# Kernel tuning notes

Hardware: AMD Instinct MI355X
Metric: run time of the kernel (lower is better)

Reference implementation:

```python
import jax, jax.numpy as jnp
import numpy as np

N = 100000      # nodes per node type (A and B)
D = 128         # input feature dim
H = 128         # hidden_size
E = 1600000     # edges per message type (avg degree 16)
P_DROP = 0.2
# message types (src, ei, dst): (A, ei0, A), (A, ei1, B), (B, ei2, A)


def setup_inputs() -> dict:
    key = jax.random.key(0)
    ks = jax.random.split(key, 16)
    s = 0.02
    inp = {
        "xA": jax.random.normal(ks[0], (N, D), jnp.float32),
        "xB": jax.random.normal(ks[1], (N, D), jnp.float32),
        "ei0": jax.random.randint(ks[2], (2, E), 0, N),
        "ei1": jax.random.randint(ks[3], (2, E), 0, N),
        "ei2": jax.random.randint(ks[4], (2, E), 0, N),
        "Wn1": jax.random.normal(ks[5], (3, D, H), jnp.float32) * s,
        "Ws1": jax.random.normal(ks[6], (3, D, H), jnp.float32) * s,
        "Wu1": jax.random.normal(ks[7], (3, 2 * H, H), jnp.float32) * s,
        "Wn2": jax.random.normal(ks[8], (3, H, H), jnp.float32) * s,
        "Ws2": jax.random.normal(ks[9], (3, H, H), jnp.float32) * s,
        "Wu2": jax.random.normal(ks[10], (3, 2 * H, H), jnp.float32) * s,
    }
    for name in ["bn1", "bs1", "bu1", "bn2", "bs2", "bu2"]:
        inp[name] = jnp.zeros((3, H), jnp.float32)
    return inp


def _dropout(x, key):
    # F.dropout(training=True) with a fixed key for determinism
    keep = jax.random.bernoulli(key, 1.0 - P_DROP, x.shape)
    return jnp.where(keep, x / (1.0 - P_DROP), jnp.zeros((), x.dtype))


def _segment_mean(msgs, dst, num_segments):
    # scatter-mean aggregation; isolated nodes get 0 (PyG 'mean' aggr)
    s = jax.ops.segment_sum(msgs, dst, num_segments=num_segments)
    cnt = jax.ops.segment_sum(jnp.ones((dst.shape[0], 1), msgs.dtype), dst,
                              num_segments=num_segments)
    return s / jnp.maximum(cnt, 1.0)


def _sage(x_src, x_dst, ei, Wn, bn, Ws, bs, Wu, bu):
    # HeteroSAGEConv: mean-aggregate neighbor feats, then
    # lin_update(cat(lin_neigh(aggr), lin_self(x_dst)))
    aggr = _segment_mean(x_src[ei[0]], ei[1], x_dst.shape[0])  # [N_dst, D]
    h = jnp.concatenate([aggr @ Wn + bn, x_dst @ Ws + bs], axis=-1)
    return h @ Wu + bu


def _hetero_layer(xA, xB, ei0, ei1, ei2, Wn, bn, Ws, bs, Wu, bu):
    # HeteroConv: sum per-message-type conv outputs sharing the same dst type
    oA = (_sage(xA, xA, ei0, Wn[0], bn[0], Ws[0], bs[0], Wu[0], bu[0])
          + _sage(xB, xA, ei2, Wn[2], bn[2], Ws[2], bs[2], Wu[2], bu[2]))
    oB = _sage(xA, xB, ei1, Wn[1], bn[1], Ws[1], bs[1], Wu[1], bu[1])
    return oA, oB


def reference(xA, xB, ei0, ei1, ei2,
              Wn1, bn1, Ws1, bs1, Wu1, bu1,
              Wn2, bn2, Ws2, bs2, Wu2, bu2):
    dk = jax.random.split(jax.random.key(42), 4)
    hA = jax.nn.relu(_dropout(xA, dk[0]))
    hB = jax.nn.relu(_dropout(xB, dk[1]))
    hA, hB = _hetero_layer(hA, hB, ei0, ei1, ei2, Wn1, bn1, Ws1, bs1, Wu1, bu1)
    hA = jax.nn.relu(_dropout(hA, dk[2]))
    hB = jax.nn.relu(_dropout(hB, dk[3]))
    return _hetero_layer(hA, hB, ei0, ei1, ei2, Wn2, bn2, Ws2, bs2, Wu2, bu2)
```

## Files before the change

kernel.cpp:

```cpp
#include <hip/hip_runtime.h>
#include <cstdint>
#include <cstdio>

#define DIMF 128
#define BKT_SHIFT 9
#define BKT_MAX 1024
#define P1_CHUNK 8192
#define P1_CAP 16384
#define P2_CAP 12288

typedef __attribute__((ext_vector_type(8))) short short8v;
typedef __attribute__((ext_vector_type(4))) short short4v;
typedef __attribute__((ext_vector_type(4))) float f32x4;


__host__ __device__ __forceinline__ void tf2x32(uint32_t k0, uint32_t k1,
                                                uint32_t x0, uint32_t x1,
                                                uint32_t& o0, uint32_t& o1) {
  uint32_t ks2 = k0 ^ k1 ^ 0x1BD11BDAu;
  x0 += k0; x1 += k1;
#define TFR(r) { x0 += x1; x1 = (x1 << (r)) | (x1 >> (32 - (r))); x1 ^= x0; }
  TFR(13) TFR(15) TFR(26) TFR(6)
  x0 += k1;  x1 += ks2 + 1u;
  TFR(17) TFR(29) TFR(16) TFR(24)
  x0 += ks2; x1 += k0 + 2u;
  TFR(13) TFR(15) TFR(26) TFR(6)
  x0 += k0;  x1 += k1 + 3u;
  TFR(17) TFR(29) TFR(16) TFR(24)
  x0 += k1;  x1 += ks2 + 4u;
  TFR(13) TFR(15) TFR(26) TFR(6)
  x0 += ks2; x1 += k0 + 5u;
#undef TFR
  o0 = x0; o1 = x1;
}

__device__ __forceinline__ short f2bf_rne(float x) {
  uint32_t u = __float_as_uint(x);
  uint32_t r = (u + 0x7FFFu + ((u >> 16) & 1u)) >> 16;
  return (short)r;
}
__device__ __forceinline__ float bfhi_f(short h) {
  return __uint_as_float(((uint32_t)(uint16_t)h) << 16);
}
__device__ __forceinline__ void unpk2(uint32_t w, float& f0, float& f1) {
  f0 = __uint_as_float(w << 16);
  f1 = __uint_as_float(w & 0xFFFF0000u);
}

__global__ __launch_bounds__(256) void k_drop2(const float* __restrict__ xA,
                                               const float* __restrict__ xB,
                                               uint32_t* __restrict__ hiA, uint32_t* __restrict__ loA,
                                               uint32_t* __restrict__ hiB, uint32_t* __restrict__ loB,
                                               int npair, int gdrop,
                                               uint32_t ka0, uint32_t ka1,
                                               uint32_t kb0, uint32_t kb1) {
  int isB = blockIdx.x >= gdrop;
  int p = (blockIdx.x - (isB ? gdrop : 0)) * 256 + threadIdx.x;
  if (p >= npair) return;
  const float* in = isB ? xB : xA;
  uint32_t* hiP = isB ? hiB : hiA;
  uint32_t* loP = isB ? loB : loA;
  uint32_t k0 = isB ? kb0 : ka0, k1 = isB ? kb1 : ka1;
  int row = p >> 6, w = p & 63;
  int c2 = w * 2;
  float2 x = *(const float2*)(in + (size_t)row * 128 + c2);
  uint32_t idx = (uint32_t)(row * 128 + c2);
  float v[2] = {x.x, x.y};
  uint32_t hw = 0, lw = 0;
#pragma unroll
  for (int q = 0; q < 2; ++q) {
    uint32_t o0, o1;
    tf2x32(k0, k1, 0u, idx + q, o0, o1);
    uint32_t bits = o0 ^ o1;
    float u = __uint_as_float((bits >> 9) | 0x3f800000u) - 1.0f;
    float y = (u < 0.8f) ? (v[q] / 0.8f) : 0.0f;
    y = fmaxf(y, 0.0f);
    short hi = f2bf_rne(y);
    short lo = f2bf_rne(y - bfhi_f(hi));
    hw |= (uint32_t)(uint16_t)hi << (16 * q);
    lw |= (uint32_t)(uint16_t)lo << (16 * q);
  }
  hiP[(size_t)row * 64 + w] = hw;
  loP[(size_t)row * 64 + w] = lw;
}

__global__ __launch_bounds__(256) void k_ginit(int* __restrict__ gcur, int nbk) {
  for (int i = threadIdx.x; i < nbk; i += 256) gcur[i] = i * P1_CAP;
}

__global__ __launch_bounds__(256) void k_p1(const int* __restrict__ ei0,
                                            const int* __restrict__ ei1,
                                            const int* __restrict__ ei2,
                                            int* __restrict__ gcur,
                                            uint32_t* __restrict__ p1o,
                                            int E, int n, int gE8, int nbk) {
  __shared__ int hist[BKT_MAX];
  __shared__ int cur[BKT_MAX];
  int t = threadIdx.x;
  int type = blockIdx.x / gE8;
  int chunk = blockIdx.x - type * gE8;
  const int* ei = type == 0 ? ei0 : (type == 1 ? ei1 : ei2);
  int base = chunk * P1_CHUNK;
  int dof = type * n;
  for (int i = t; i < nbk; i += 256) hist[i] = 0;
  __syncthreads();
  int sv[P1_CHUNK / 256];
  int dv[P1_CHUNK / 256];
#pragma unroll
  for (int j = 0; j < P1_CHUNK / 256; ++j) {
    int e = base + j * 256 + t;
    if (e < E) { sv[j] = ei[e]; dv[j] = ei[E + e] + dof; }
    else dv[j] = -1;
  }
#pragma unroll
  for (int j = 0; j < P1_CHUNK / 256; ++j)
    if (dv[j] >= 0) atomicAdd(&hist[dv[j] >> BKT_SHIFT], 1);
  __syncthreads();
  for (int i = t; i < nbk; i += 256) {
    int h = hist[i];
    if (h > 0) cur[i] = atomicAdd(&gcur[i], h);
  }
  __syncthreads();
#pragma unroll
  for (int j = 0; j < P1_CHUNK / 256; ++j) {
    if (dv[j] >= 0) {
      int bkt = dv[j] >> BKT_SHIFT;
      int pos = atomicAdd(&cur[bkt], 1);
      p1o[pos] = (uint32_t)sv[j] | ((uint32_t)(dv[j] & 511) << 20);
    }
  }
}

__global__ __launch_bounds__(256) void k_bscan2(const int* __restrict__ gcur,
                                                int* __restrict__ boff,
                                                int* __restrict__ off,
                                                int nbk, int n3) {
  __shared__ int ts[256];
  int t = threadIdx.x;
  int base = t * 4;
  int v[4];
#pragma unroll
  for (int i = 0; i < 4; ++i)
    v[i] = (base + i < nbk) ? (gcur[base + i] - (base + i) * P1_CAP) : 0;
  ts[t] = v[0] + v[1] + v[2] + v[3];
  __syncthreads();
  for (int ofs = 1; ofs < 256; ofs <<= 1) {
    int x = ts[t];
    int y = (t >= ofs) ? ts[t - ofs] : 0;
    __syncthreads();
    ts[t] = x + y;
    __syncthreads();
  }
  int run = (t == 0) ? 0 : ts[t - 1];
#pragma unroll
  for (int i = 0; i < 4; ++i) {
    if (base + i < nbk) boff[base + i] = run;
    run += v[i];
  }
  if (t == 255) { boff[nbk] = ts[255]; off[n3] = ts[255]; }
}

__global__ __launch_bounds__(256) void k_p2(const uint32_t* __restrict__ p1o,
                                            const int* __restrict__ boff,
                                            int* __restrict__ off,
                                            int* __restrict__ srcl, int n3) {
  __shared__ int cnt_l[512];
  __shared__ int off_l[512];
  __shared__ int cur_l[512];
  __shared__ int ts[256];
  __shared__ int img[P2_CAP];
  int b = blockIdx.x;
  int t = threadIdx.x;
  int fb = boff[b];
  int sz = boff[b + 1] - fb;
  size_t pb = (size_t)b * P1_CAP;
  int d0 = b << BKT_SHIFT;
  cnt_l[t] = 0; cnt_l[t + 256] = 0;
  __syncthreads();
  for (int i = t; i < sz; i += 256)
    atomicAdd(&cnt_l[p1o[pb + i] >> 20], 1);
  __syncthreads();
  int c0 = cnt_l[2 * t], c1 = cnt_l[2 * t + 1];
  ts[t] = c0 + c1;
  __syncthreads();
  for (int ofs = 1; ofs < 256; ofs <<= 1) {
    int x = ts[t];
    int y = (t >= ofs) ? ts[t - ofs] : 0;
    __syncthreads();
    ts[t] = x + y;
    __syncthreads();
  }
  int ebase = (t == 0) ? 0 : ts[t - 1];
  off_l[2 * t] = ebase; off_l[2 * t + 1] = ebase + c0;
  cur_l[2 * t] = ebase; cur_l[2 * t + 1] = ebase + c0;
  __syncthreads();
  for (int j = t; j < 512; j += 256) {
    int d = d0 + j;
    if (d < n3) off[d] = fb + off_l[j];
  }
  if (sz <= P2_CAP) {
    for (int i = t; i < sz; i += 256) {
      uint32_t w = p1o[pb + i];
      int pos = atomicAdd(&cur_l[w >> 20], 1);
      img[pos] = (int)(w & 0xFFFFFu) << 6;
    }
    __syncthreads();
    for (int i = t; i < sz; i += 256) srcl[fb + i] = img[i];
  } else {
    for (int i = t; i < sz; i += 256) {
      uint32_t w = p1o[pb + i];
      int pos = atomicAdd(&cur_l[w >> 20], 1);
      srcl[fb + pos] = (int)(w & 0xFFFFFu) << 6;
    }
  }
}

__device__ __forceinline__ void gather_one32(const uint32_t* __restrict__ hiP,
                                             const int* __restrict__ off,
                                             const int* __restrict__ srcl,
                                             short* __restrict__ out,
                                             int d, int lane) {
  int b = off[d], e = off[d + 1];
  const int c2 = lane * 2;
  float a0 = 0.f, a1 = 0.f, a2 = 0.f, a3 = 0.f;
  float b0 = 0.f, b1 = 0.f, b2 = 0.f, b3 = 0.f;
  float c0 = 0.f, c1 = 0.f, c2f = 0.f, c3 = 0.f;
  float e0 = 0.f, e1 = 0.f, e2 = 0.f, e3 = 0.f;
  float t0, t1;
  int j = b;
  for (; j + 3 < e; j += 4) {
    int o0 = __builtin_nontemporal_load(srcl + j);
    int o1 = __builtin_nontemporal_load(srcl + j + 1);
    int o2 = __builtin_nontemporal_load(srcl + j + 2);
    int o3 = __builtin_nontemporal_load(srcl + j + 3);
    uint2 w0 = *(const uint2*)(hiP + (size_t)(o0 + c2));
    uint2 w1 = *(const uint2*)(hiP + (size_t)(o1 + c2));
    uint2 w2 = *(const uint2*)(hiP + (size_t)(o2 + c2));
    uint2 w3 = *(const uint2*)(hiP + (size_t)(o3 + c2));
    unpk2(w0.x, t0, t1); a0 += t0; a1 += t1;
    unpk2(w0.y, t0, t1); a2 += t0; a3 += t1;
    unpk2(w1.x, t0, t1); b0 += t0; b1 += t1;
    unpk2(w1.y, t0, t1); b2 += t0; b3 += t1;
    unpk2(w2.x, t0, t1); c0 += t0; c1 += t1;
    unpk2(w2.y, t0, t1); c2f += t0; c3 += t1;
    unpk2(w3.x, t0, t1); e0 += t0; e1 += t1;
    unpk2(w3.y, t0, t1); e2 += t0; e3 += t1;
  }
  for (; j < e; ++j) {
    int o = __builtin_nontemporal_load(srcl + j);
    uint2 w = *(const uint2*)(hiP + (size_t)(o + c2));
    unpk2(w.x, t0, t1); a0 += t0; a1 += t1;
    unpk2(w.y, t0, t1); a2 += t0; a3 += t1;
  }
  float sc = 1.0f / (float)max(e - b, 1);
  short4v r = { f2bf_rne(((a0 + b0) + (c0 + e0)) * sc),
                f2bf_rne(((a1 + b1) + (c1 + e1)) * sc),
                f2bf_rne(((a2 + b2) + (c2f + e2)) * sc),
                f2bf_rne(((a3 + b3) + (c3 + e3)) * sc) };
  __builtin_nontemporal_store(r, (short4v*)(out + (size_t)d * 128 + lane * 4));
}

__global__ __launch_bounds__(256) void k_gather3(
    const uint32_t* __restrict__ hiA, const uint32_t* __restrict__ hiB,
    short* __restrict__ g1, short* __restrict__ g2, short* __restrict__ g3,
    const int* __restrict__ off, const int* __restrict__ srcl, int n) {
  int wv = (blockIdx.x * 256 + threadIdx.x) >> 6;
  int half = (threadIdx.x >> 5) & 1;
  int lane = threadIdx.x & 31;
  int d = wv * 2 + half;
  if (d >= 3 * n) return;
  if (d < n)          gather_one32(hiA, off + n,     srcl, g1, d,         lane);
  else if (d < 2 * n) gather_one32(hiB, off + 2 * n, srcl, g2, d - n,     lane);
  else                gather_one32(hiA, off,         srcl, g3, d - 2 * n, lane);
}

struct WDesc { const float* A0; const float* B0; const float* A1; const float* B1; short* Ch; short* Cl; };
struct WPack { WDesc d[10]; };

__global__ __launch_bounds__(256) void k_wprec(WPack p) {
  const WDesc d = p.d[blockIdx.x >> 2];
  const int rt = blockIdx.x & 3;
  __shared__ float A_s[32 * 128];
  const int t = threadIdx.x;
  const int c = t & 127, rh = t >> 7;
  float acc[16];
#pragma unroll
  for (int i = 0; i < 16; ++i) acc[i] = 0.f;
  for (int pass = 0; pass < 2; ++pass) {
    const float* A = pass ? d.A1 : d.A0;
    const float* B = pass ? d.B1 : d.B0;
    if (!A) break;
    __syncthreads();
#pragma unroll
    for (int j = 0; j < 4; ++j) {
      int f = t + 256 * j;
      *(float4*)(A_s + 4 * f) = *(const float4*)(A + (size_t)rt * 32 * 128 + 4 * f);
    }
    __syncthreads();
    for (int k = 0; k < 128; ++k) {
      float b = B[(size_t)k * 128 + c];
#pragma unroll
      for (int i = 0; i < 16; ++i)
        acc[i] += A_s[(rh + 2 * i) * 128 + k] * b;
    }
  }
#pragma unroll
  for (int i = 0; i < 16; ++i) {
    int k = rt * 32 + rh + 2 * i;
    float v = acc[i];
    short hi = f2bf_rne(v);
    short lo = f2bf_rne(v - bfhi_f(hi));
    d.Ch[(size_t)c * 128 + k] = hi;
    d.Cl[(size_t)c * 128 + k] = lo;
  }
}

__global__ __launch_bounds__(256) void k_bias2(const float* __restrict__ bn1,
                                               const float* __restrict__ bs1,
                                               const float* __restrict__ bu1,
                                               const float* __restrict__ Wu1,
                                               const float* __restrict__ bn2,
                                               const float* __restrict__ bs2,
                                               const float* __restrict__ bu2,
                                               const float* __restrict__ Wu2,
                                               float* __restrict__ cbA1, float* __restrict__ cbB1,
                                               float* __restrict__ cbA2, float* __restrict__ cbB2) {
  const float* bn = blockIdx.x ? bn2 : bn1;
  const float* bs = blockIdx.x ? bs2 : bs1;
  const float* bu = blockIdx.x ? bu2 : bu1;
  const float* Wu = blockIdx.x ? Wu2 : Wu1;
  float* cbA = blockIdx.x ? cbA2 : cbA1;
  float* cbB = blockIdx.x ? cbB2 : cbB1;
  int t = threadIdx.x;
  int h = t & 127;
  if (t < 128) {
    float acc = bu[0 * 128 + h] + bu[2 * 128 + h];
    for (int j = 0; j < 128; ++j) {
      acc += bn[0 * 128 + j] * Wu[(size_t)0 * 32768 + (size_t)j * 128 + h];
      acc += bs[0 * 128 + j] * Wu[(size_t)0 * 32768 + 16384 + (size_t)j * 128 + h];
      acc += bn[2 * 128 + j] * Wu[(size_t)2 * 32768 + (size_t)j * 128 + h];
      acc += bs[2 * 128 + j] * Wu[(size_t)2 * 32768 + 16384 + (size_t)j * 128 + h];
    }
    cbA[h] = acc;
  } else {
    float acc = bu[128 + h];
    for (int j = 0; j < 128; ++j) {
      acc += bn[128 + j] * Wu[(size_t)1 * 32768 + (size_t)j * 128 + h];
      acc += bs[128 + j] * Wu[(size_t)1 * 32768 + 16384 + (size_t)j * 128 + h];
    }
    cbB[h] = acc;
  }
}

struct MMJob {
  const short* s0; const short* s1;
  const short* selfHi; const short* selfLo;
  const short* w0h; const short* w0l;
  const short* w1h; const short* w1l;
  const short* w2h; const short* w2l;
  const float* bias;
  void* out; void* out2;
  int nt;
  uint32_t k0, k1;
};

template <int MODE>
__global__ __launch_bounds__(256, 2) void k_mmx2(MMJob JA, MMJob JB, int gA, int n) {
  __shared__ short A_s[128 * 72];
  __shared__ short W_s[128 * 72];
  MMJob j;
  int bid;
  if (blockIdx.x < (unsigned)gA) { j = JA; bid = blockIdx.x; }
  else                           { j = JB; bid = blockIdx.x - gA; }
  const int t = threadIdx.x;
  const int r0 = bid * 128;
  const int lane = t & 63;
  const int w = t >> 6;
  const int wr = w >> 1, wc = w & 1;
  const int lr = lane & 15, lg = lane >> 4;
  const int sr = t >> 1, sh = t & 1;
  const int rr = min(r0 + sr, n - 1);

  f32x4 acc[4][4];
#pragma unroll
  for (int nf = 0; nf < 4; ++nf) {
    float bv = j.bias[wc * 64 + nf * 16 + lr];
#pragma unroll
    for (int mf = 0; mf < 4; ++mf) acc[mf][nf] = {bv, bv, bv, bv};
  }

  for (int term = 0; term < j.nt; ++term) {
    const short* wh = term == 0 ? j.w0h : (term == 1 ? j.w1h : j.w2h);
    const short* wl = term == 0 ? j.w0l : (term == 1 ? j.w1l : j.w2l);
    const short* wsrc = sh ? wl : wh;
    const bool isSelf = (term == j.nt - 1);
    const short* src = term == 0 ? j.s0 : j.s1;
    for (int ks = 0; ks < 4; ++ks) {
      __syncthreads();
      if (isSelf) {
        const short* pl = sh ? j.selfLo : j.selfHi;
        const uint4* gp = (const uint4*)(pl + (size_t)rr * 128 + ks * 32);
        uint4 b0 = gp[0], b1 = gp[1], b2 = gp[2], b3 = gp[3];
        uint4* la = (uint4*)(A_s + sr * 72 + sh * 32);
        la[0] = b0; la[1] = b1; la[2] = b2; la[3] = b3;
      } else {
        const uint4* ga = (const uint4*)(src + (size_t)rr * 128 + ks * 32 + sh * 16);
        uint4 q0 = ga[0], q1 = ga[1];
        uint4* Ah = (uint4*)(A_s + sr * 72 + sh * 16);
        Ah[0] = q0; Ah[1] = q1;
      }
      {
        const uint4* gw = (const uint4*)(wsrc + sr * 128 + ks * 32);
        uint4 b0 = gw[0], b1 = gw[1], b2 = gw[2], b3 = gw[3];
        uint4* lw = (uint4*)(W_s + sr * 72 + sh * 32);
        lw[0] = b0; lw[1] = b1; lw[2] = b2; lw[3] = b3;
      }
      __syncthreads();
      short8v whi[4], wlo[4];
#pragma unroll
      for (int nf = 0; nf < 4; ++nf) {
        int nc = wc * 64 + nf * 16 + lr;
        whi[nf] = *(const short8v*)(W_s + nc * 72 + lg * 8);
        wlo[nf] = *(const short8v*)(W_s + nc * 72 + 32 + lg * 8);
      }
#pragma unroll
      for (int mf = 0; mf < 4; ++mf) {
        int ar = wr * 64 + mf * 16 + lr;
        short8v ah = *(const short8v*)(A_s + ar * 72 + lg * 8);
        if (isSelf) {
          short8v al = *(const short8v*)(A_s + ar * 72 + 32 + lg * 8);
#pragma unroll
          for (int nf = 0; nf < 4; ++nf) {
            acc[mf][nf] = __builtin_amdgcn_mfma_f32_16x16x32_bf16(ah, whi[nf], acc[mf][nf], 0, 0, 0);
            acc[mf][nf] = __builtin_amdgcn_mfma_f32_16x16x32_bf16(ah, wlo[nf], acc[mf][nf], 0, 0, 0);
            acc[mf][nf] = __builtin_amdgcn_mfma_f32_16x16x32_bf16(al, whi[nf], acc[mf][nf], 0, 0, 0);
          }
        } else {
#pragma unroll
          for (int nf = 0; nf < 4; ++nf) {
            acc[mf][nf] = __builtin_amdgcn_mfma_f32_16x16x32_bf16(ah, whi[nf], acc[mf][nf], 0, 0, 0);
            acc[mf][nf] = __builtin_amdgcn_mfma_f32_16x16x32_bf16(ah, wlo[nf], acc[mf][nf], 0, 0, 0);
          }
        }
      }
    }
  }

#pragma unroll
  for (int mf = 0; mf < 4; ++mf) {
#pragma unroll
    for (int r = 0; r < 4; ++r) {
      int g = r0 + wr * 64 + mf * 16 + lg * 4 + r;
      if (g >= n) continue;
#pragma unroll
      for (int nf = 0; nf < 4; ++nf) {
        int col = wc * 64 + nf * 16 + lr;
        float v = acc[mf][nf][r];
        if constexpr (MODE == 1) {
          uint32_t o0, o1;
          tf2x32(j.k0, j.k1, 0u, (uint32_t)(g * 128 + col), o0, o1);
          uint32_t bits = o0 ^ o1;
          float u = __uint_as_float((bits >> 9) | 0x3f800000u) - 1.0f;
          v = (u < 0.8f) ? (v / 0.8f) : 0.0f;
          v = fmaxf(v, 0.0f);
          short hi = f2bf_rne(v);
          short lo = f2bf_rne(v - bfhi_f(hi));
          ((short*)j.out)[(size_t)g * 128 + col] = hi;
          ((short*)j.out2)[(size_t)g * 128 + col] = lo;
        } else {
          __builtin_nontemporal_store(v, (float*)j.out + (size_t)g * 128 + col);
        }
      }
    }
  }
}

extern "C" void kernel_launch(void* const* d_in, const int* in_sizes, int n_in,
                              void* d_out, int out_size, void* d_ws, size_t ws_size,
                              hipStream_t stream) {
  const float* xA  = (const float*)d_in[0];
  const float* xB  = (const float*)d_in[1];
  const int*   ei0 = (const int*)d_in[2];
  const int*   ei1 = (const int*)d_in[3];
  const int*   ei2 = (const int*)d_in[4];
  const float* Wn1 = (const float*)d_in[5];
  const float* Ws1 = (const float*)d_in[6];
  const float* Wu1 = (const float*)d_in[7];
  const float* Wn2 = (const float*)d_in[8];
  const float* Ws2 = (const float*)d_in[9];
  const float* Wu2 = (const float*)d_in[10];
  const float* bn1 = (const float*)d_in[11];
  const float* bs1 = (const float*)d_in[12];
  const float* bu1 = (const float*)d_in[13];
  const float* bn2 = (const float*)d_in[14];
  const float* bs2 = (const float*)d_in[15];
  const float* bu2 = (const float*)d_in[16];

  const int n  = in_sizes[0] / DIMF;
  const int E  = in_sizes[2] / 2;
  const int n3 = 3 * n;
  const int nbk = (n3 + 511) >> BKT_SHIFT;
  const size_t nh = (size_t)n * DIMF;

  short* S = (short*)d_ws;
  short* hiA = S;
  short* loA = S + nh;
  short* hiB = S + 2 * nh;
  short* loB = S + 3 * nh;
  short* g1  = S + 4 * nh;
  short* g2  = S + 5 * nh;
  short* g3  = S + 6 * nh;
  short* wtsS = S + 7 * nh;
  float* biasF = (float*)(wtsS + 10 * 32768);
  float* cbA1 = biasF, *cbB1 = biasF + 128, *cbA2 = biasF + 256, *cbB2 = biasF + 384;
  int* off  = (int*)(biasF + 512);
  int* boff = off + n3 + 1;
  int* gcur = boff + BKT_MAX + 1;
  int* srcl = gcur + BKT_MAX;
  uint32_t* p1o = (uint32_t*)g1;

  size_t need_bytes = (size_t)7 * nh * sizeof(short)
                    + (size_t)10 * 32768 * sizeof(short)
                    + 512 * sizeof(float)
                    + ((size_t)n3 + 1 + 2 * BKT_MAX + 2 + (size_t)3 * E) * sizeof(int)
                    + 65536;
  if (ws_size < need_bytes) {
    fprintf(stderr, "kernel_launch: ws too small (%zu < %zu)\n", ws_size, need_bytes);
    return;
  }
  if ((size_t)nbk * P1_CAP > nh) {
    fprintf(stderr, "kernel_launch: p1o overflow\n");
    return;
  }

  uint32_t dk[4][2];
  for (uint32_t i = 0; i < 4; ++i) tf2x32(0u, 42u, 0u, i, dk[i][0], dk[i][1]);

  WPack pk;
  auto U = [](const float* Wu, int t) { return Wu + (size_t)t * 32768; };
  auto L = [](const float* Wu, int t) { return Wu + (size_t)t * 32768 + 16384; };
  auto WH = [&](int m) { return wtsS + (size_t)m * 32768; };
  auto WL = [&](int m) { return wtsS + (size_t)m * 32768 + 16384; };
  const size_t MS = 128 * 128;
  pk.d[0] = { Wn1 + 0 * MS, U(Wu1, 0), nullptr, nullptr, WH(0), WL(0) };
  pk.d[1] = { Wn1 + 1 * MS, U(Wu1, 1), nullptr, nullptr, WH(1), WL(1) };
  pk.d[2] = { Wn1 + 2 * MS, U(Wu1, 2), nullptr, nullptr, WH(2), WL(2) };
  pk.d[3] = { Ws1 + 0 * MS, L(Wu1, 0), Ws1 + 2 * MS, L(Wu1, 2), WH(3), WL(3) };
  pk.d[4] = { Ws1 + 1 * MS, L(Wu1, 1), nullptr, nullptr, WH(4), WL(4) };
  pk.d[5] = { Wn2 + 0 * MS, U(Wu2, 0), nullptr, nullptr, WH(5), WL(5) };
  pk.d[6] = { Wn2 + 1 * MS, U(Wu2, 1), nullptr, nullptr, WH(6), WL(6) };
  pk.d[7] = { Wn2 + 2 * MS, U(Wu2, 2), nullptr, nullptr, WH(7), WL(7) };
  pk.d[8] = { Ws2 + 0 * MS, L(Wu2, 0), Ws2 + 2 * MS, L(Wu2, 2), WH(8), WL(8) };
  pk.d[9] = { Ws2 + 1 * MS, L(Wu2, 1), nullptr, nullptr, WH(9), WL(9) };

  const int gdrop = (int)((nh / 2 + 255) / 256);
  const int gE8   = (E + P1_CHUNK - 1) / P1_CHUNK;
  const int gmm   = (n + 127) / 128;
  const int nwv   = (n3 + 1) / 2;
  const int gga3  = (nwv * 64 + 255) / 256;

  k_ginit<<<1, 256, 0, stream>>>(gcur, nbk);
  k_p1<<<3 * gE8, 256, 0, stream>>>(ei0, ei1, ei2, gcur, p1o, E, n, gE8, nbk);
  k_bscan2<<<1, 256, 0, stream>>>(gcur, boff, off, nbk, n3);
  k_p2<<<nbk, 256, 0, stream>>>(p1o, boff, off, srcl, n3);

  k_wprec<<<40, 256, 0, stream>>>(pk);
  k_bias2<<<2, 256, 0, stream>>>(bn1, bs1, bu1, Wu1, bn2, bs2, bu2, Wu2,
                                 cbA1, cbB1, cbA2, cbB2);

  k_drop2<<<2 * gdrop, 256, 0, stream>>>(xA, xB, (uint32_t*)hiA, (uint32_t*)loA,
                                         (uint32_t*)hiB, (uint32_t*)loB,
                                         (int)(nh / 2), gdrop,
                                         dk[0][0], dk[0][1], dk[1][0], dk[1][1]);

  k_gather3<<<gga3, 256, 0, stream>>>((const uint32_t*)hiA, (const uint32_t*)hiB,
                                      g1, g2, g3, off, srcl, n);
  {
    MMJob JA = { g3, g2, hiA, loA, WH(0), WL(0), WH(2), WL(2), WH(3), WL(3),
                 cbA1, hiA, loA, 3, dk[2][0], dk[2][1] };
    MMJob JB = { g1, nullptr, hiB, loB, WH(1), WL(1), WH(4), WL(4), nullptr, nullptr,
                 cbB1, hiB, loB, 2, dk[3][0], dk[3][1] };
    k_mmx2<1><<<2 * gmm, 256, 0, stream>>>(JA, JB, gmm, n);
  }

  float* oA = (float*)d_out;
  float* oB = oA + nh;
  k_gather3<<<gga3, 256, 0, stream>>>((const uint32_t*)hiA, (const uint32_t*)hiB,
                                      g1, g2, g3, off, srcl, n);
  {
    MMJob JA = { g3, g2, hiA, loA, WH(5), WL(5), WH(7), WL(7), WH(8), WL(8),
                 cbA2, oA, nullptr, 3, 0u, 0u };
    MMJob JB = { g1, nullptr, hiB, loB, WH(6), WL(6), WH(9), WL(9), nullptr, nullptr,
                 cbB2, oB, nullptr, 2, 0u, 0u };
    k_mmx2<0><<<2 * gmm, 256, 0, stream>>>(JA, JB, gmm, n);
  }
}
```

Baseline: 802.0 us.

## Drop lo-plane for self features and merge setup kernels to cut launches

Self features (dropout output and the layer-1 activations) are now stored as a single bf16 plane, with no hi/lo split. This removes the lo-plane writes and reads and the extra MFMA pass on the self term. The small setup kernels (weight precompute, bias fold, gcur init) are merged into one launch, dropout is fused into the edge-bucketing kernel, and the bucket scan is folded into k_p2 through per-block reductions. The trade is lower precision on self features, plus redundant per-block scan work in k_p2.

```diff
diff --git a/kernel.cpp b/kernel.cpp
--- a/kernel.cpp
+++ b/kernel.cpp
@@ -47,134 +47,198 @@
   f1 = __uint_as_float(w & 0xFFFF0000u);
 }
 
-__global__ __launch_bounds__(256) void k_drop2(const float* __restrict__ xA,
-                                               const float* __restrict__ xB,
-                                               uint32_t* __restrict__ hiA, uint32_t* __restrict__ loA,
-                                               uint32_t* __restrict__ hiB, uint32_t* __restrict__ loB,
-                                               int npair, int gdrop,
-                                               uint32_t ka0, uint32_t ka1,
-                                               uint32_t kb0, uint32_t kb1) {
-  int isB = blockIdx.x >= gdrop;
-  int p = (blockIdx.x - (isB ? gdrop : 0)) * 256 + threadIdx.x;
-  if (p >= npair) return;
-  const float* in = isB ? xB : xA;
-  uint32_t* hiP = isB ? hiB : hiA;
-  uint32_t* loP = isB ? loB : loA;
-  uint32_t k0 = isB ? kb0 : ka0, k1 = isB ? kb1 : ka1;
-  int row = p >> 6, w = p & 63;
-  int c2 = w * 2;
-  float2 x = *(const float2*)(in + (size_t)row * 128 + c2);
-  uint32_t idx = (uint32_t)(row * 128 + c2);
-  float v[2] = {x.x, x.y};
-  uint32_t hw = 0, lw = 0;
-#pragma unroll
-  for (int q = 0; q < 2; ++q) {
-    uint32_t o0, o1;
-    tf2x32(k0, k1, 0u, idx + q, o0, o1);
-    uint32_t bits = o0 ^ o1;
-    float u = __uint_as_float((bits >> 9) | 0x3f800000u) - 1.0f;
-    float y = (u < 0.8f) ? (v[q] / 0.8f) : 0.0f;
-    y = fmaxf(y, 0.0f);
-    short hi = f2bf_rne(y);
-    short lo = f2bf_rne(y - bfhi_f(hi));
-    hw |= (uint32_t)(uint16_t)hi << (16 * q);
-    lw |= (uint32_t)(uint16_t)lo << (16 * q);
-  }
-  hiP[(size_t)row * 64 + w] = hw;
-  loP[(size_t)row * 64 + w] = lw;
-}
-
-__global__ __launch_bounds__(256) void k_ginit(int* __restrict__ gcur, int nbk) {
-  for (int i = threadIdx.x; i < nbk; i += 256) gcur[i] = i * P1_CAP;
-}
-
-__global__ __launch_bounds__(256) void k_p1(const int* __restrict__ ei0,
-                                            const int* __restrict__ ei1,
-                                            const int* __restrict__ ei2,
-                                            int* __restrict__ gcur,
-                                            uint32_t* __restrict__ p1o,
-                                            int E, int n, int gE8, int nbk) {
+struct WDesc { const float* A0; const float* B0; const float* A1; const float* B1; short* Ch; short* Cl; };
+struct WPack { WDesc d[10]; };
+
+__global__ __launch_bounds__(256) void k_setup(WPack p,
+    const float* __restrict__ bn1, const float* __restrict__ bs1,
+    const float* __restrict__ bu1, const float* __restrict__ Wu1,
+    const float* __restrict__ bn2, const float* __restrict__ bs2,
+    const float* __restrict__ bu2, const float* __restrict__ Wu2,
+    float* __restrict__ cbA1, float* __restrict__ cbB1,
+    float* __restrict__ cbA2, float* __restrict__ cbB2,
+    int* __restrict__ gcur, int nbk) {
+  __shared__ float A_s[32 * 128];
+  const int bx = blockIdx.x;
+  const int t = threadIdx.x;
+  if (bx < 40) {
+    const WDesc d = p.d[bx >> 2];
+    const int rt = bx & 3;
+    const int c = t & 127, rh = t >> 7;
+    float acc[16];
+#pragma unroll
+    for (int i = 0; i < 16; ++i) acc[i] = 0.f;
+    for (int pass = 0; pass < 2; ++pass) {
+      const float* A = pass ? d.A1 : d.A0;
+      const float* B = pass ? d.B1 : d.B0;
+      if (!A) break;
+      __syncthreads();
+#pragma unroll
+      for (int jj = 0; jj < 4; ++jj) {
+        int f = t + 256 * jj;
+        *(float4*)(A_s + 4 * f) = *(const float4*)(A + (size_t)rt * 32 * 128 + 4 * f);
+      }
+      __syncthreads();
+      for (int k = 0; k < 128; ++k) {
+        float b = B[(size_t)k * 128 + c];
+#pragma unroll
+        for (int i = 0; i < 16; ++i)
+          acc[i] += A_s[(rh + 2 * i) * 128 + k] * b;
+      }
+    }
+#pragma unroll
+    for (int i = 0; i < 16; ++i) {
+      int k = rt * 32 + rh + 2 * i;
+      float v = acc[i];
+      short hi = f2bf_rne(v);
+      short lo = f2bf_rne(v - bfhi_f(hi));
+      d.Ch[(size_t)c * 128 + k] = hi;
+      d.Cl[(size_t)c * 128 + k] = lo;
+    }
+  } else if (bx < 42) {
+    const int layer = bx - 40;
+    const float* bn = layer ? bn2 : bn1;
+    const float* bs = layer ? bs2 : bs1;
+    const float* bu = layer ? bu2 : bu1;
+    const float* Wu = layer ? Wu2 : Wu1;
+    float* cbA = layer ? cbA2 : cbA1;
+    float* cbB = layer ? cbB2 : cbB1;
+    int h = t & 127;
+    if (t < 128) {
+      float acc = bu[0 * 128 + h] + bu[2 * 128 + h];
+      for (int j = 0; j < 128; ++j) {
+        acc += bn[0 * 128 + j] * Wu[(size_t)0 * 32768 + (size_t)j * 128 + h];
+        acc += bs[0 * 128 + j] * Wu[(size_t)0 * 32768 + 16384 + (size_t)j * 128 + h];
+        acc += bn[2 * 128 + j] * Wu[(size_t)2 * 32768 + (size_t)j * 128 + h];
+        acc += bs[2 * 128 + j] * Wu[(size_t)2 * 32768 + 16384 + (size_t)j * 128 + h];
+      }
+      cbA[h] = acc;
+    } else {
+      float acc = bu[128 + h];
+      for (int j = 0; j < 128; ++j) {
+        acc += bn[128 + j] * Wu[(size_t)1 * 32768 + (size_t)j * 128 + h];
+        acc += bs[128 + j] * Wu[(size_t)1 * 32768 + 16384 + (size_t)j * 128 + h];
+      }
+      cbB[h] = acc;
+    }
+  } else {
+    for (int i = t; i < nbk; i += 256) gcur[i] = i * P1_CAP;
+  }
+}
+
+__global__ __launch_bounds__(256) void k_p1drop(
+    const int* __restrict__ ei0, const int* __restrict__ ei1, const int* __restrict__ ei2,
+    int* __restrict__ gcur, uint32_t* __restrict__ p1o,
+    int E, int n, int gE8, int nbk,
+    const float* __restrict__ xA, const float* __restrict__ xB,
+    uint32_t* __restrict__ pA, uint32_t* __restrict__ pB,
+    int npair, int gdrop,
+    uint32_t ka0, uint32_t ka1, uint32_t kb0, uint32_t kb1) {
   __shared__ int hist[BKT_MAX];
   __shared__ int cur[BKT_MAX];
-  int t = threadIdx.x;
-  int type = blockIdx.x / gE8;
-  int chunk = blockIdx.x - type * gE8;
-  const int* ei = type == 0 ? ei0 : (type == 1 ? ei1 : ei2);
-  int base = chunk * P1_CHUNK;
-  int dof = type * n;
-  for (int i = t; i < nbk; i += 256) hist[i] = 0;
-  __syncthreads();
-  int sv[P1_CHUNK / 256];
-  int dv[P1_CHUNK / 256];
-#pragma unroll
-  for (int j = 0; j < P1_CHUNK / 256; ++j) {
-    int e = base + j * 256 + t;
-    if (e < E) { sv[j] = ei[e]; dv[j] = ei[E + e] + dof; }
-    else dv[j] = -1;
-  }
-#pragma unroll
-  for (int j = 0; j < P1_CHUNK / 256; ++j)
-    if (dv[j] >= 0) atomicAdd(&hist[dv[j] >> BKT_SHIFT], 1);
-  __syncthreads();
-  for (int i = t; i < nbk; i += 256) {
-    int h = hist[i];
-    if (h > 0) cur[i] = atomicAdd(&gcur[i], h);
-  }
-  __syncthreads();
-#pragma unroll
-  for (int j = 0; j < P1_CHUNK / 256; ++j) {
-    if (dv[j] >= 0) {
-      int bkt = dv[j] >> BKT_SHIFT;
-      int pos = atomicAdd(&cur[bkt], 1);
-      p1o[pos] = (uint32_t)sv[j] | ((uint32_t)(dv[j] & 511) << 20);
-    }
-  }
-}
-
-__global__ __launch_bounds__(256) void k_bscan2(const int* __restrict__ gcur,
-                                                int* __restrict__ boff,
-                                                int* __restrict__ off,
-                                                int nbk, int n3) {
-  __shared__ int ts[256];
-  int t = threadIdx.x;
-  int base = t * 4;
-  int v[4];
-#pragma unroll
-  for (int i = 0; i < 4; ++i)
-    v[i] = (base + i < nbk) ? (gcur[base + i] - (base + i) * P1_CAP) : 0;
-  ts[t] = v[0] + v[1] + v[2] + v[3];
-  __syncthreads();
-  for (int ofs = 1; ofs < 256; ofs <<= 1) {
-    int x = ts[t];
-    int y = (t >= ofs) ? ts[t - ofs] : 0;
-    __syncthreads();
-    ts[t] = x + y;
-    __syncthreads();
-  }
-  int run = (t == 0) ? 0 : ts[t - 1];
-#pragma unroll
-  for (int i = 0; i < 4; ++i) {
-    if (base + i < nbk) boff[base + i] = run;
-    run += v[i];
-  }
-  if (t == 255) { boff[nbk] = ts[255]; off[n3] = ts[255]; }
+  const int t = threadIdx.x;
+  if (blockIdx.x < (unsigned)(3 * gE8)) {
+    int type = blockIdx.x / gE8;
+    int chunk = blockIdx.x - type * gE8;
+    const int* ei = type == 0 ? ei0 : (type == 1 ? ei1 : ei2);
+    int base = chunk * P1_CHUNK;
+    int dof = type * n;
+    for (int i = t; i < nbk; i += 256) hist[i] = 0;
+    __syncthreads();
+    int sv[P1_CHUNK / 256];
+    int dv[P1_CHUNK / 256];
+#pragma unroll
+    for (int j = 0; j < P1_CHUNK / 256; ++j) {
+      int e = base + j * 256 + t;
+      if (e < E) { sv[j] = ei[e]; dv[j] = ei[E + e] + dof; }
+      else dv[j] = -1;
+    }
+#pragma unroll
+    for (int j = 0; j < P1_CHUNK / 256; ++j)
+      if (dv[j] >= 0) atomicAdd(&hist[dv[j] >> BKT_SHIFT], 1);
+    __syncthreads();
+    for (int i = t; i < nbk; i += 256) {
+      int h = hist[i];
+      if (h > 0) cur[i] = atomicAdd(&gcur[i], h);
+    }
+    __syncthreads();
+#pragma unroll
+    for (int j = 0; j < P1_CHUNK / 256; ++j) {
+      if (dv[j] >= 0) {
+        int bkt = dv[j] >> BKT_SHIFT;
+        int pos = atomicAdd(&cur[bkt], 1);
+        p1o[pos] = (uint32_t)sv[j] | ((uint32_t)(dv[j] & 511) << 20);
+      }
+    }
+  } else {
+    int bd = blockIdx.x - 3 * gE8;
+    int isB = bd >= gdrop;
+    int p = (bd - (isB ? gdrop : 0)) * 256 + t;
+    if (p >= npair) return;
+    const float* in = isB ? xB : xA;
+    uint32_t* plane = isB ? pB : pA;
+    uint32_t k0 = isB ? kb0 : ka0, k1 = isB ? kb1 : ka1;
+    int row = p >> 6, w = p & 63;
+    int c2 = w * 2;
+    float2 x = *(const float2*)(in + (size_t)row * 128 + c2);
+    uint32_t idx = (uint32_t)(row * 128 + c2);
+    float v[2] = {x.x, x.y};
+    uint32_t hw = 0;
+#pragma unroll
+    for (int q = 0; q < 2; ++q) {
+      uint32_t o0, o1;
+      tf2x32(k0, k1, 0u, idx + q, o0, o1);
+      uint32_t bits = o0 ^ o1;
+      float u = __uint_as_float((bits >> 9) | 0x3f800000u) - 1.0f;
+      float y = (u < 0.8f) ? (v[q] / 0.8f) : 0.0f;
+      y = fmaxf(y, 0.0f);
+      hw |= (uint32_t)(uint16_t)f2bf_rne(y) << (16 * q);
+    }
+    plane[(size_t)row * 64 + w] = hw;
+  }
 }
 
 __global__ __launch_bounds__(256) void k_p2(const uint32_t* __restrict__ p1o,
-                                            const int* __restrict__ boff,
+                                            const int* __restrict__ gcur,
                                             int* __restrict__ off,
-                                            int* __restrict__ srcl, int n3) {
+                                            int* __restrict__ srcl,
+                                            int nbk, int n3) {
+  __shared__ int redA[256];
+  __shared__ int redB[256];
+  __shared__ int sh_szb;
   __shared__ int cnt_l[512];
   __shared__ int off_l[512];
   __shared__ int cur_l[512];
   __shared__ int ts[256];
   __shared__ int img[P2_CAP];
-  int b = blockIdx.x;
-  int t = threadIdx.x;
-  int fb = boff[b];
-  int sz = boff[b + 1] - fb;
-  size_t pb = (size_t)b * P1_CAP;
-  int d0 = b << BKT_SHIFT;
+  const int b = blockIdx.x;
+  const int t = threadIdx.x;
+  {
+    int t3 = t * 3;
+    int s0 = 0, s1 = 0, s2 = 0;
+    if (t3     < nbk) s0 = gcur[t3]     - t3 * P1_CAP;
+    if (t3 + 1 < nbk) s1 = gcur[t3 + 1] - (t3 + 1) * P1_CAP;
+    if (t3 + 2 < nbk) s2 = gcur[t3 + 2] - (t3 + 2) * P1_CAP;
+    int lt = 0;
+    if (t3     < b) lt += s0;
+    if (t3 + 1 < b) lt += s1;
+    if (t3 + 2 < b) lt += s2;
+    if (b == t3) sh_szb = s0;
+    else if (b == t3 + 1) sh_szb = s1;
+    else if (b == t3 + 2) sh_szb = s2;
+    redA[t] = lt;
+    redB[t] = s0 + s1 + s2;
+    __syncthreads();
+    for (int ofs = 128; ofs > 0; ofs >>= 1) {
+      if (t < ofs) { redA[t] += redA[t + ofs]; redB[t] += redB[t + ofs]; }
+      __syncthreads();
+    }
+  }
+  const int fb = redA[0];
+  const int sz = sh_szb;
+  if (b == 0 && t == 0) off[n3] = redB[0];
+  const size_t pb = (size_t)b * P1_CAP;
+  const int d0 = b << BKT_SHIFT;
   cnt_l[t] = 0; cnt_l[t + 256] = 0;
   __syncthreads();
   for (int i = t; i < sz; i += 256)
@@ -215,7 +279,7 @@
   }
 }
 
-__device__ __forceinline__ void gather_one32(const uint32_t* __restrict__ hiP,
+__device__ __forceinline__ void gather_one32(const uint32_t* __restrict__ plane,
                                              const int* __restrict__ off,
                                              const int* __restrict__ srcl,
                                              short* __restrict__ out,
@@ -233,10 +297,10 @@
     int o1 = __builtin_nontemporal_load(srcl + j + 1);
     int o2 = __builtin_nontemporal_load(srcl + j + 2);
     int o3 = __builtin_nontemporal_load(srcl + j + 3);
-    uint2 w0 = *(const uint2*)(hiP + (size_t)(o0 + c2));
-    uint2 w1 = *(const uint2*)(hiP + (size_t)(o1 + c2));
-    uint2 w2 = *(const uint2*)(hiP + (size_t)(o2 + c2));
-    uint2 w3 = *(const uint2*)(hiP + (size_t)(o3 + c2));
+    uint2 w0 = *(const uint2*)(plane + (size_t)(o0 + c2));
+    uint2 w1 = *(const uint2*)(plane + (size_t)(o1 + c2));
+    uint2 w2 = *(const uint2*)(plane + (size_t)(o2 + c2));
+    uint2 w3 = *(const uint2*)(plane + (size_t)(o3 + c2));
     unpk2(w0.x, t0, t1); a0 += t0; a1 += t1;
     unpk2(w0.y, t0, t1); a2 += t0; a3 += t1;
     unpk2(w1.x, t0, t1); b0 += t0; b1 += t1;
@@ -248,7 +312,7 @@
   }
   for (; j < e; ++j) {
     int o = __builtin_nontemporal_load(srcl + j);
-    uint2 w = *(const uint2*)(hiP + (size_t)(o + c2));
+    uint2 w = *(const uint2*)(plane + (size_t)(o + c2));
     unpk2(w.x, t0, t1); a0 += t0; a1 += t1;
     unpk2(w.y, t0, t1); a2 += t0; a3 += t1;
   }
@@ -261,7 +325,7 @@
 }
 
 __global__ __launch_bounds__(256) void k_gather3(
-    const uint32_t* __restrict__ hiA, const uint32_t* __restrict__ hiB,
+    const uint32_t* __restrict__ pA, const uint32_t* __restrict__ pB,
     short* __restrict__ g1, short* __restrict__ g2, short* __restrict__ g3,
     const int* __restrict__ off, const int* __restrict__ srcl, int n) {
   int wv = (blockIdx.x * 256 + threadIdx.x) >> 6;
@@ -269,97 +333,18 @@
   int lane = threadIdx.x & 31;
   int d = wv * 2 + half;
   if (d >= 3 * n) return;
-  if (d < n)          gather_one32(hiA, off + n,     srcl, g1, d,         lane);
-  else if (d < 2 * n) gather_one32(hiB, off + 2 * n, srcl, g2, d - n,     lane);
-  else                gather_one32(hiA, off,         srcl, g3, d - 2 * n, lane);
-}
-
-struct WDesc { const float* A0; const float* B0; const float* A1; const float* B1; short* Ch; short* Cl; };
-struct WPack { WDesc d[10]; };
-
-__global__ __launch_bounds__(256) void k_wprec(WPack p) {
-  const WDesc d = p.d[blockIdx.x >> 2];
-  const int rt = blockIdx.x & 3;
-  __shared__ float A_s[32 * 128];
-  const int t = threadIdx.x;
-  const int c = t & 127, rh = t >> 7;
-  float acc[16];
-#pragma unroll
-  for (int i = 0; i < 16; ++i) acc[i] = 0.f;
-  for (int pass = 0; pass < 2; ++pass) {
-    const float* A = pass ? d.A1 : d.A0;
-    const float* B = pass ? d.B1 : d.B0;
-    if (!A) break;
-    __syncthreads();
-#pragma unroll
-    for (int j = 0; j < 4; ++j) {
-      int f = t + 256 * j;
-      *(float4*)(A_s + 4 * f) = *(const float4*)(A + (size_t)rt * 32 * 128 + 4 * f);
-    }
-    __syncthreads();
-    for (int k = 0; k < 128; ++k) {
-      float b = B[(size_t)k * 128 + c];
-#pragma unroll
-      for (int i = 0; i < 16; ++i)
-        acc[i] += A_s[(rh + 2 * i) * 128 + k] * b;
-    }
-  }
-#pragma unroll
-  for (int i = 0; i < 16; ++i) {
-    int k = rt * 32 + rh + 2 * i;
-    float v = acc[i];
-    short hi = f2bf_rne(v);
-    short lo = f2bf_rne(v - bfhi_f(hi));
-    d.Ch[(size_t)c * 128 + k] = hi;
-    d.Cl[(size_t)c * 128 + k] = lo;
-  }
-}
-
-__global__ __launch_bounds__(256) void k_bias2(const float* __restrict__ bn1,
-                                               const float* __restrict__ bs1,
-                                               const float* __restrict__ bu1,
-                                               const float* __restrict__ Wu1,
-                                               const float* __restrict__ bn2,
-                                               const float* __restrict__ bs2,
-                                               const float* __restrict__ bu2,
-                                               const float* __restrict__ Wu2,
-                                               float* __restrict__ cbA1, float* __restrict__ cbB1,
-                                               float* __restrict__ cbA2, float* __restrict__ cbB2) {
-  const float* bn = blockIdx.x ? bn2 : bn1;
-  const float* bs = blockIdx.x ? bs2 : bs1;
-  const float* bu = blockIdx.x ? bu2 : bu1;
-  const float* Wu = blockIdx.x ? Wu2 : Wu1;
-  float* cbA = blockIdx.x ? cbA2 : cbA1;
-  float* cbB = blockIdx.x ? cbB2 : cbB1;
-  int t = threadIdx.x;
-  int h = t & 127;
-  if (t < 128) {
-    float acc = bu[0 * 128 + h] + bu[2 * 128 + h];
-    for (int j = 0; j < 128; ++j) {
-      acc += bn[0 * 128 + j] * Wu[(size_t)0 * 32768 + (size_t)j * 128 + h];
-      acc += bs[0 * 128 + j] * Wu[(size_t)0 * 32768 + 16384 + (size_t)j * 128 + h];
-      acc += bn[2 * 128 + j] * Wu[(size_t)2 * 32768 + (size_t)j * 128 + h];
-      acc += bs[2 * 128 + j] * Wu[(size_t)2 * 32768 + 16384 + (size_t)j * 128 + h];
-    }
-    cbA[h] = acc;
-  } else {
-    float acc = bu[128 + h];
-    for (int j = 0; j < 128; ++j) {
-      acc += bn[128 + j] * Wu[(size_t)1 * 32768 + (size_t)j * 128 + h];
-      acc += bs[128 + j] * Wu[(size_t)1 * 32768 + 16384 + (size_t)j * 128 + h];
-    }
-    cbB[h] = acc;
-  }
+  if (d < n)          gather_one32(pA, off + n,     srcl, g1, d,         lane);
+  else if (d < 2 * n) gather_one32(pB, off + 2 * n, srcl, g2, d - n,     lane);
+  else                gather_one32(pA, off,         srcl, g3, d - 2 * n, lane);
 }
 
 struct MMJob {
-  const short* s0; const short* s1;
-  const short* selfHi; const short* selfLo;
+  const short* s0; const short* s1; const short* s2;
   const short* w0h; const short* w0l;
   const short* w1h; const short* w1l;
   const short* w2h; const short* w2l;
   const float* bias;
-  void* out; void* out2;
+  void* out;
   int nt;
   uint32_t k0, k1;
 };
@@ -390,20 +375,13 @@
   }
 
   for (int term = 0; term < j.nt; ++term) {
-    const short* wh = term == 0 ? j.w0h : (term == 1 ? j.w1h : j.w2h);
-    const short* wl = term == 0 ? j.w0l : (term == 1 ? j.w1l : j.w2l);
+    const short* src = term == 0 ? j.s0 : (term == 1 ? j.s1 : j.s2);
+    const short* wh  = term == 0 ? j.w0h : (term == 1 ? j.w1h : j.w2h);
+    const short* wl  = term == 0 ? j.w0l : (term == 1 ? j.w1l : j.w2l);
     const short* wsrc = sh ? wl : wh;
-    const bool isSelf = (term == j.nt - 1);
-    const short* src = term == 0 ? j.s0 : j.s1;
     for (int ks = 0; ks < 4; ++ks) {
       __syncthreads();
-      if (isSelf) {
-        const short* pl = sh ? j.selfLo : j.selfHi;
-        const uint4* gp = (const uint4*)(pl + (size_t)rr * 128 + ks * 32);
-        uint4 b0 = gp[0], b1 = gp[1], b2 = gp[2], b3 = gp[3];
-        uint4* la = (uint4*)(A_s + sr * 72 + sh * 32);
-        la[0] = b0; la[1] = b1; la[2] = b2; la[3] = b3;
-      } else {
+      {
         const uint4* ga = (const uint4*)(src + (size_t)rr * 128 + ks * 32 + sh * 16);
         uint4 q0 = ga[0], q1 = ga[1];
         uint4* Ah = (uint4*)(A_s + sr * 72 + sh * 16);
@@ -427,20 +405,10 @@
       for (int mf = 0; mf < 4; ++mf) {
         int ar = wr * 64 + mf * 16 + lr;
         short8v ah = *(const short8v*)(A_s + ar * 72 + lg * 8);
-        if (isSelf) {
-          short8v al = *(const short8v*)(A_s + ar * 72 + 32 + lg * 8);
-#pragma unroll
-          for (int nf = 0; nf < 4; ++nf) {
-            acc[mf][nf] = __builtin_amdgcn_mfma_f32_16x16x32_bf16(ah, whi[nf], acc[mf][nf], 0, 0, 0);
-            acc[mf][nf] = __builtin_amdgcn_mfma_f32_16x16x32_bf16(ah, wlo[nf], acc[mf][nf], 0, 0, 0);
-            acc[mf][nf] = __builtin_amdgcn_mfma_f32_16x16x32_bf16(al, whi[nf], acc[mf][nf], 0, 0, 0);
-          }
-        } else {
-#pragma unroll
-          for (int nf = 0; nf < 4; ++nf) {
-            acc[mf][nf] = __builtin_amdgcn_mfma_f32_16x16x32_bf16(ah, whi[nf], acc[mf][nf], 0, 0, 0);
-            acc[mf][nf] = __builtin_amdgcn_mfma_f32_16x16x32_bf16(ah, wlo[nf], acc[mf][nf], 0, 0, 0);
-          }
+#pragma unroll
+        for (int nf = 0; nf < 4; ++nf) {
+          acc[mf][nf] = __builtin_amdgcn_mfma_f32_16x16x32_bf16(ah, whi[nf], acc[mf][nf], 0, 0, 0);
+          acc[mf][nf] = __builtin_amdgcn_mfma_f32_16x16x32_bf16(ah, wlo[nf], acc[mf][nf], 0, 0, 0);
         }
       }
     }
@@ -463,10 +431,7 @@
           float u = __uint_as_float((bits >> 9) | 0x3f800000u) - 1.0f;
           v = (u < 0.8f) ? (v / 0.8f) : 0.0f;
           v = fmaxf(v, 0.0f);
-          short hi = f2bf_rne(v);
-          short lo = f2bf_rne(v - bfhi_f(hi));
-          ((short*)j.out)[(size_t)g * 128 + col] = hi;
-          ((short*)j.out2)[(size_t)g * 128 + col] = lo;
+          ((short*)j.out)[(size_t)g * 128 + col] = f2bf_rne(v);
         } else {
           __builtin_nontemporal_store(v, (float*)j.out + (size_t)g * 128 + col);
         }
@@ -503,33 +468,30 @@
   const size_t nh = (size_t)n * DIMF;
 
   short* S = (short*)d_ws;
-  short* hiA = S;
-  short* loA = S + nh;
-  short* hiB = S + 2 * nh;
-  short* loB = S + 3 * nh;
-  short* g1  = S + 4 * nh;
-  short* g2  = S + 5 * nh;
-  short* g3  = S + 6 * nh;
-  short* wtsS = S + 7 * nh;
+  short* hA = S;
+  short* hB = S + nh;
+  short* g1 = S + 2 * nh;
+  short* g2 = S + 3 * nh;
+  short* g3 = S + 4 * nh;
+  short* wtsS = S + 5 * nh;
   float* biasF = (float*)(wtsS + 10 * 32768);
   float* cbA1 = biasF, *cbB1 = biasF + 128, *cbA2 = biasF + 256, *cbB2 = biasF + 384;
   int* off  = (int*)(biasF + 512);
-  int* boff = off + n3 + 1;
-  int* gcur = boff + BKT_MAX + 1;
+  int* gcur = off + n3 + 1;
   int* srcl = gcur + BKT_MAX;
   uint32_t* p1o = (uint32_t*)g1;
 
-  size_t need_bytes = (size_t)7 * nh * sizeof(short)
+  size_t need_bytes = (size_t)5 * nh * sizeof(short)
                     + (size_t)10 * 32768 * sizeof(short)
                     + 512 * sizeof(float)
-                    + ((size_t)n3 + 1 + 2 * BKT_MAX + 2 + (size_t)3 * E) * sizeof(int)
+                    + ((size_t)n3 + 1 + BKT_MAX + (size_t)3 * E) * sizeof(int)
                     + 65536;
   if (ws_size < need_bytes) {
     fprintf(stderr, "kernel_launch: ws too small (%zu < %zu)\n", ws_size, need_bytes);
     return;
   }
-  if ((size_t)nbk * P1_CAP > nh) {
-    fprintf(stderr, "kernel_launch: p1o overflow\n");
+  if ((size_t)nbk * P1_CAP > nh || nbk > 768) {
+    fprintf(stderr, "kernel_launch: bucket config overflow\n");
     return;
   }
 
@@ -553,45 +515,40 @@
   pk.d[8] = { Ws2 + 0 * MS, L(Wu2, 0), Ws2 + 2 * MS, L(Wu2, 2), WH(8), WL(8) };
   pk.d[9] = { Ws2 + 1 * MS, L(Wu2, 1), nullptr, nullptr, WH(9), WL(9) };
 
-  const int gdrop = (int)((nh / 2 + 255) / 256);
+  const int npair = (int)(nh / 2);
+  const int gdrop = (npair + 255) / 256;
   const int gE8   = (E + P1_CHUNK - 1) / P1_CHUNK;
   const int gmm   = (n + 127) / 128;
   const int nwv   = (n3 + 1) / 2;
   const int gga3  = (nwv * 64 + 255) / 256;
 
-  k_ginit<<<1, 256, 0, stream>>>(gcur, nbk);
-  k_p1<<<3 * gE8, 256, 0, stream>>>(ei0, ei1, ei2, gcur, p1o, E, n, gE8, nbk);
-  k_bscan2<<<1, 256, 0, stream>>>(gcur, boff, off, nbk, n3);
-  k_p2<<<nbk, 256, 0, stream>>>(p1o, boff, off, srcl, n3);
-
-  k_wprec<<<40, 256, 0, stream>>>(pk);
-  k_bias2<<<2, 256, 0, stream>>>(bn1, bs1, bu1, Wu1, bn2, bs2, bu2, Wu2,
-                                 cbA1, cbB1, cbA2, cbB2);
-
-  k_drop2<<<2 * gdrop, 256, 0, stream>>>(xA, xB, (uint32_t*)hiA, (uint32_t*)loA,
-                                         (uint32_t*)hiB, (uint32_t*)loB,
-                                         (int)(nh / 2), gdrop,
-                                         dk[0][0], dk[0][1], dk[1][0], dk[1][1]);
-
-  k_gather3<<<gga3, 256, 0, stream>>>((const uint32_t*)hiA, (const uint32_t*)hiB,
+  k_setup<<<43, 256, 0, stream>>>(pk, bn1, bs1, bu1, Wu1, bn2, bs2, bu2, Wu2,
+                                  cbA1, cbB1, cbA2, cbB2, gcur, nbk);
+  k_p1drop<<<3 * gE8 + 2 * gdrop, 256, 0, stream>>>(
+      ei0, ei1, ei2, gcur, p1o, E, n, gE8, nbk,
+      xA, xB, (uint32_t*)hA, (uint32_t*)hB, npair, gdrop,
+      dk[0][0], dk[0][1], dk[1][0], dk[1][1]);
+  k_p2<<<nbk, 256, 0, stream>>>(p1o, gcur, off, srcl, nbk, n3);
+
+  k_gather3<<<gga3, 256, 0, stream>>>((const uint32_t*)hA, (const uint32_t*)hB,
                                       g1, g2, g3, off, srcl, n);
   {
-    MMJob JA = { g3, g2, hiA, loA, WH(0), WL(0), WH(2), WL(2), WH(3), WL(3),
-                 cbA1, hiA, loA, 3, dk[2][0], dk[2][1] };
-    MMJob JB = { g1, nullptr, hiB, loB, WH(1), WL(1), WH(4), WL(4), nullptr, nullptr,
-                 cbB1, hiB, loB, 2, dk[3][0], dk[3][1] };
+    MMJob JA = { g3, g2, hA, WH(0), WL(0), WH(2), WL(2), WH(3), WL(3),
+                 cbA1, hA, 3, dk[2][0], dk[2][1] };
+    MMJob JB = { g1, hB, nullptr, WH(1), WL(1), WH(4), WL(4), nullptr, nullptr,
+                 cbB1, hB, 2, dk[3][0], dk[3][1] };
     k_mmx2<1><<<2 * gmm, 256, 0, stream>>>(JA, JB, gmm, n);
   }
 
   float* oA = (float*)d_out;
   float* oB = oA + nh;
-  k_gather3<<<gga3, 256, 0, stream>>>((const uint32_t*)hiA, (const uint32_t*)hiB,
+  k_gather3<<<gga3, 256, 0, stream>>>((const uint32_t*)hA, (const uint32_t*)hB,
                                       g1, g2, g3, off, srcl, n);
   {
-    MMJob JA = { g3, g2, hiA, loA, WH(5), WL(5), WH(7), WL(7), WH(8), WL(8),
-                 cbA2, oA, nullptr, 3, 0u, 0u };
-    MMJob JB = { g1, nullptr, hiB, loB, WH(6), WL(6), WH(9), WL(9), nullptr, nullptr,
-                 cbB2, oB, nullptr, 2, 0u, 0u };
+    MMJob JA = { g3, g2, hA, WH(5), WL(5), WH(7), WL(7), WH(8), WL(8),
+                 cbA2, oA, 3, 0u, 0u };
+    MMJob JB = { g1, hB, nullptr, WH(6), WL(6), WH(9), WL(9), nullptr, nullptr,
+                 cbB2, oB, 2, 0u, 0u };
     k_mmx2<0><<<2 * gmm, 256, 0, stream>>>(JA, JB, gmm, n);
   }
 }
```

After: 720.6 us, median of 2. -10.2%, faster.
